# Kernel tuning notes

Measured on AMD Instinct MI355X. Metric: run time of the kernel, lower is better.

## Reference

```python
import jax, jax.numpy as jnp
import numpy as np

N_NODES = 100000


def gcn_conv(x, W, b, src, dst, n_nodes):
    """PyG GCNConv: out = D^{-1/2} (A + I) D^{-1/2} X W + b."""
    h = x @ W  # [N, F_out]
    # add self-loops
    loop = jnp.arange(n_nodes, dtype=src.dtype)
    s = jnp.concatenate([src, loop])
    d = jnp.concatenate([dst, loop])
    # symmetric normalization (deg counts incoming edges incl. self-loop)
    deg = jax.ops.segment_sum(jnp.ones_like(d, dtype=h.dtype), d, num_segments=n_nodes)
    dinv = jnp.where(deg > 0, jax.lax.rsqrt(deg), 0.0)
    coef = dinv[s] * dinv[d]  # [E+N]
    msg = h[s] * coef[:, None]  # gather + scale
    out = jax.ops.segment_sum(msg, d, num_segments=n_nodes)  # scatter-add
    return out + b


def setup_inputs() -> dict:
    key = jax.random.key(0)
    k1, k2, k3, k4, k5, k6 = jax.random.split(key, 6)
    in_dim, hidden_dim, out_dim = 128, 64, 64
    n_edges = 1000000
    x = jax.random.normal(k1, (N_NODES, in_dim), dtype=jnp.float32)
    edge_index = jax.random.randint(k2, (2, n_edges), 0, N_NODES, dtype=jnp.int64)
    # glorot-style init for GCN weights
    W1 = jax.random.normal(k3, (in_dim, hidden_dim), dtype=jnp.float32) / np.sqrt(in_dim)
    b1 = jnp.zeros((hidden_dim,), dtype=jnp.float32)
    W2 = jax.random.normal(k4, (hidden_dim, out_dim), dtype=jnp.float32) / np.sqrt(hidden_dim)
    b2 = jnp.zeros((out_dim,), dtype=jnp.float32)
    return {"x": x, "edge_index": edge_index, "W1": W1, "b1": b1, "W2": W2, "b2": b2}


def reference(x, edge_index, W1, b1, W2, b2):
    src, dst = edge_index[0], edge_index[1]
    h = jax.nn.relu(gcn_conv(x, W1, b1, src, dst, N_NODES))
    out = gcn_conv(h, W2, b2, src, dst, N_NODES)
    return out
```

## Files before the change

kernel.cpp:

```cpp
#include <hip/hip_runtime.h>


#define MD 48
#define FILLB 8192

typedef __attribute__((ext_vector_type(8))) short bf16x8;
typedef __attribute__((ext_vector_type(4))) float f32x4;
typedef __attribute__((ext_vector_type(4))) int   i32x4;
typedef __attribute__((ext_vector_type(4))) unsigned u32x4;

__device__ inline float bf2f(unsigned short v) {
    unsigned u = (unsigned)v << 16;
    return __builtin_bit_cast(float, u);
}
__device__ inline unsigned short f2bf(float f) {
    unsigned u = __builtin_bit_cast(unsigned, f);
    unsigned r = (u + 0x7FFFu + ((u >> 16) & 1u)) >> 16;
    return (unsigned short)r;
}

__device__ inline void convW_one(const float* __restrict__ W, short* __restrict__ Wth,
                                 short* __restrict__ Wtl, int K, int k, int f) {
    float v = W[k * 64 + f];
    unsigned b = __builtin_bit_cast(unsigned, v);
    unsigned hb = b & 0xFFFF0000u;
    float d = v - __builtin_bit_cast(float, hb);
    unsigned lb = __builtin_bit_cast(unsigned, d);
    Wth[f * K + k] = (short)(hb >> 16);
    Wtl[f * K + k] = (short)(lb >> 16);
}

__global__ __launch_bounds__(256) void k_prep(int* __restrict__ cnt, int n, int nbz,
                                              const float* __restrict__ W1,
                                              short* __restrict__ W1th, short* __restrict__ W1tl,
                                              const float* __restrict__ W2,
                                              short* __restrict__ W2th, short* __restrict__ W2tl) {
    const int b = blockIdx.x;
    if (b < nbz) {
        int i = b * 256 + threadIdx.x;
        if (i < n) cnt[i] = 0;
    } else if (b < nbz + 128) {
        if (threadIdx.x < 64) convW_one(W1, W1th, W1tl, 128, b - nbz, threadIdx.x);
    } else {
        if (threadIdx.x < 64) convW_one(W2, W2th, W2tl, 64, b - nbz - 128, threadIdx.x);
    }
}

template <int K>
__device__ inline void mm_f32A_body(int bid, const float* __restrict__ X,
                                    const short* __restrict__ Wth,
                                    const short* __restrict__ Wtl,
                                    unsigned short* __restrict__ G, int n) {
    const int lane = threadIdx.x & 63;
    const int w = threadIdx.x >> 6;
    const int r0 = lane & 15;
    const int kq = lane >> 4;
    const int arow = bid * 64 + w * 16 + r0;
    const float* xrow = X + (size_t)(arow < n ? arow : n - 1) * K;

    f32x4 acc[4] = {};
#pragma unroll
    for (int kc = 0; kc < K / 32; ++kc) {
        const int ks = kc * 32 + kq * 8;
        float xv[8];
        *(f32x4*)&xv[0] = __builtin_nontemporal_load((const f32x4*)&xrow[ks]);
        *(f32x4*)&xv[4] = __builtin_nontemporal_load((const f32x4*)&xrow[ks + 4]);
        bf16x8 ah, al;
#pragma unroll
        for (int j = 0; j < 8; ++j) {
            unsigned b = __builtin_bit_cast(unsigned, xv[j]);
            unsigned hb = b & 0xFFFF0000u;
            float d = xv[j] - __builtin_bit_cast(float, hb);
            unsigned lb = __builtin_bit_cast(unsigned, d);
            ah[j] = (short)(hb >> 16);
            al[j] = (short)(lb >> 16);
        }
#pragma unroll
        for (int c = 0; c < 4; ++c) {
            bf16x8 bh = *(const bf16x8*)&Wth[(c * 16 + r0) * K + ks];
            bf16x8 bl = *(const bf16x8*)&Wtl[(c * 16 + r0) * K + ks];
            acc[c] = __builtin_amdgcn_mfma_f32_16x16x32_bf16(ah, bh, acc[c], 0, 0, 0);
            acc[c] = __builtin_amdgcn_mfma_f32_16x16x32_bf16(ah, bl, acc[c], 0, 0, 0);
            acc[c] = __builtin_amdgcn_mfma_f32_16x16x32_bf16(al, bh, acc[c], 0, 0, 0);
        }
    }
    const int orow = bid * 64 + w * 16 + kq * 4;
#pragma unroll
    for (int rg = 0; rg < 4; ++rg) {
        int gr = orow + rg;
        if (gr < n) {
#pragma unroll
            for (int c = 0; c < 4; ++c)
                G[(size_t)gr * 64 + c * 16 + r0] = f2bf(acc[c][rg]);
        }
    }
}

template <int K>
__global__ __launch_bounds__(256) void k_fill_mm1(const int* __restrict__ src,
                                                  const int* __restrict__ dst, int E,
                                                  int* __restrict__ cnt,
                                                  int* __restrict__ col_ell, int npx,
                                                  const float* __restrict__ X,
                                                  const short* __restrict__ Wth,
                                                  const short* __restrict__ Wtl,
                                                  unsigned short* __restrict__ G, int n) {
    if (blockIdx.x < FILLB) {
        const int myxcd = blockIdx.x & 7;
        const int lo = myxcd * npx;
        const int hi = lo + npx;
        const int vb = blockIdx.x >> 3;
        const int nvb = FILLB >> 3;
        const int tid = vb * 256 + threadIdx.x;
        const int nthr = nvb * 256;
        for (int base = tid * 4; base < E; base += nthr * 4) {
            i32x4 d4 = __builtin_nontemporal_load((const i32x4*)&dst[base]);
#pragma unroll
            for (int k = 0; k < 4; ++k) {
                int d = d4[k];
                if (d >= lo && d < hi) {
                    int p = atomicAdd(&cnt[d], 1);
                    if (p < MD)
                        col_ell[(size_t)d * MD + p] = __builtin_nontemporal_load(&src[base + k]);
                }
            }
        }
    } else {
        mm_f32A_body<K>(blockIdx.x - FILLB, X, Wth, Wtl, G, n);
    }
}

__global__ __launch_bounds__(256) void k_mm_bf16A(const unsigned short* __restrict__ A,
                                                  const short* __restrict__ Wth,
                                                  const short* __restrict__ Wtl,
                                                  unsigned short* __restrict__ G, int n) {
    constexpr int K = 64;
    const int lane = threadIdx.x & 63;
    const int w = threadIdx.x >> 6;
    const int r0 = lane & 15;
    const int kq = lane >> 4;
    const int arow = blockIdx.x * 64 + w * 16 + r0;
    const unsigned short* ar = A + (size_t)(arow < n ? arow : n - 1) * K;

    f32x4 acc[4] = {};
#pragma unroll
    for (int kc = 0; kc < K / 32; ++kc) {
        const int ks = kc * 32 + kq * 8;
        bf16x8 a = __builtin_nontemporal_load((const bf16x8*)&ar[ks]);
#pragma unroll
        for (int c = 0; c < 4; ++c) {
            bf16x8 bh = *(const bf16x8*)&Wth[(c * 16 + r0) * K + ks];
            bf16x8 bl = *(const bf16x8*)&Wtl[(c * 16 + r0) * K + ks];
            acc[c] = __builtin_amdgcn_mfma_f32_16x16x32_bf16(a, bh, acc[c], 0, 0, 0);
            acc[c] = __builtin_amdgcn_mfma_f32_16x16x32_bf16(a, bl, acc[c], 0, 0, 0);
        }
    }
    const int orow = blockIdx.x * 64 + w * 16 + kq * 4;
#pragma unroll
    for (int rg = 0; rg < 4; ++rg) {
        int gr = orow + rg;
        if (gr < n) {
#pragma unroll
            for (int c = 0; c < 4; ++c)
                G[(size_t)gr * 64 + c * 16 + r0] = f2bf(acc[c][rg]);
        }
    }
}

template <bool RELU, bool OUTBF>
__global__ __launch_bounds__(256) void k_gather8(const unsigned short* __restrict__ g,
                                                 const int* __restrict__ cntArr,
                                                 const int* __restrict__ col_ell,
                                                 const float* __restrict__ bias,
                                                 void* __restrict__ dest, int n) {
    const int node = blockIdx.x * 4 + (threadIdx.x >> 6);
    if (node >= n) return;
    const int lane = threadIdx.x & 63;
    const int grp = lane >> 3;
    const int fl = lane & 7;
    const int cn = cntArr[node];
    const int lc = min(cn, MD);
    const float dn = rsqrtf((float)(cn + 1));
    const int myidx = __builtin_nontemporal_load(&col_ell[(size_t)node * MD + lane]);
    const int vidx = (lane < lc) ? myidx : node;
    const float mydv = rsqrtf((float)(cntArr[vidx] + 1));

    float acc[8] = {};
    if (grp == 0) {
        u32x4 u = *(const u32x4*)&g[(size_t)node * 64 + fl * 8];
        acc[0] = dn * bf2f((unsigned short)(u[0] & 0xFFFF));
        acc[1] = dn * bf2f((unsigned short)(u[0] >> 16));
        acc[2] = dn * bf2f((unsigned short)(u[1] & 0xFFFF));
        acc[3] = dn * bf2f((unsigned short)(u[1] >> 16));
        acc[4] = dn * bf2f((unsigned short)(u[2] & 0xFFFF));
        acc[5] = dn * bf2f((unsigned short)(u[2] >> 16));
        acc[6] = dn * bf2f((unsigned short)(u[3] & 0xFFFF));
        acc[7] = dn * bf2f((unsigned short)(u[3] >> 16));
    }
    for (int j8 = 0; j8 < lc; j8 += 8) {
        int j = j8 + grp;
        int s = __shfl(myidx, j);
        float ds = __shfl(mydv, j);
        if (j < lc) {
            u32x4 u = *(const u32x4*)&g[(size_t)s * 64 + fl * 8];
            acc[0] = fmaf(ds, bf2f((unsigned short)(u[0] & 0xFFFF)), acc[0]);
            acc[1] = fmaf(ds, bf2f((unsigned short)(u[0] >> 16)),    acc[1]);
            acc[2] = fmaf(ds, bf2f((unsigned short)(u[1] & 0xFFFF)), acc[2]);
            acc[3] = fmaf(ds, bf2f((unsigned short)(u[1] >> 16)),    acc[3]);
            acc[4] = fmaf(ds, bf2f((unsigned short)(u[2] & 0xFFFF)), acc[4]);
            acc[5] = fmaf(ds, bf2f((unsigned short)(u[2] >> 16)),    acc[5]);
            acc[6] = fmaf(ds, bf2f((unsigned short)(u[3] & 0xFFFF)), acc[6]);
            acc[7] = fmaf(ds, bf2f((unsigned short)(u[3] >> 16)),    acc[7]);
        }
    }
#pragma unroll
    for (int k = 0; k < 8; ++k) {
        acc[k] += __shfl_xor(acc[k], 8);
        acc[k] += __shfl_xor(acc[k], 16);
        acc[k] += __shfl_xor(acc[k], 32);
    }
    if (grp == 0) {
        float v[8];
        const float* bv = &bias[fl * 8];
#pragma unroll
        for (int k = 0; k < 8; ++k) {
            v[k] = fmaf(acc[k], dn, bv[k]);
            if (RELU) v[k] = fmaxf(v[k], 0.f);
        }
        if (OUTBF) {
            u32x4 o;
            o[0] = (unsigned)f2bf(v[0]) | ((unsigned)f2bf(v[1]) << 16);
            o[1] = (unsigned)f2bf(v[2]) | ((unsigned)f2bf(v[3]) << 16);
            o[2] = (unsigned)f2bf(v[4]) | ((unsigned)f2bf(v[5]) << 16);
            o[3] = (unsigned)f2bf(v[6]) | ((unsigned)f2bf(v[7]) << 16);
            __builtin_nontemporal_store(o, (u32x4*)&((unsigned short*)dest)[(size_t)node * 64 + fl * 8]);
        } else {
            float* dp = &((float*)dest)[(size_t)node * 64 + fl * 8];
            __builtin_nontemporal_store(*(const f32x4*)&v[0], (f32x4*)&dp[0]);
            __builtin_nontemporal_store(*(const f32x4*)&v[4], (f32x4*)&dp[4]);
        }
    }
}

extern "C" void kernel_launch(void* const* d_in, const int* in_sizes, int n_in,
                              void* d_out, int out_size, void* d_ws, size_t ws_size,
                              hipStream_t stream) {
    const float* x  = (const float*)d_in[0];
    const int*   ei = (const int*)d_in[1];
    const float* W1 = (const float*)d_in[2];
    const float* b1 = (const float*)d_in[3];
    const float* W2 = (const float*)d_in[4];
    const float* b2 = (const float*)d_in[5];

    const int N = in_sizes[0] / 128;
    const int E = in_sizes[1] / 2;
    const int* src = ei;
    const int* dst = ei + E;
    float* out = (float*)d_out;

    char* ws = (char*)d_ws;
    size_t off = 0;
    auto alloc = [&](size_t bytes) {
        void* p = ws + off;
        off += (bytes + 63) & ~(size_t)63;
        return p;
    };
    unsigned short* a1   = (unsigned short*)alloc((size_t)N * 64 * 2);
    unsigned short* gbuf = (unsigned short*)alloc((size_t)N * 64 * 2);
    int*   cnt     = (int*)alloc((size_t)N * 4);
    int*   col_ell = (int*)alloc(((size_t)N * MD + 64) * 4);
    short* W1th    = (short*)alloc((size_t)64 * 128 * 2);
    short* W1tl    = (short*)alloc((size_t)64 * 128 * 2);
    short* W2th    = (short*)alloc((size_t)64 * 64 * 2);
    short* W2tl    = (short*)alloc((size_t)64 * 64 * 2);

    const int NBZ   = (N + 255) / 256;
    const int NB_MM = (N + 63) / 64;
    const int NB_G  = (N + 3) / 4;
    const int npx   = (N + 7) / 8;

    k_prep<<<NBZ + 192, 256, 0, stream>>>(cnt, N, NBZ, W1, W1th, W1tl, W2, W2th, W2tl);

    k_fill_mm1<128><<<FILLB + NB_MM, 256, 0, stream>>>(src, dst, E, cnt, col_ell, npx,
                                                       x, W1th, W1tl, gbuf, N);

    k_gather8<true, true><<<NB_G, 256, 0, stream>>>(gbuf, cnt, col_ell, b1, a1, N);

    k_mm_bf16A<<<NB_MM, 256, 0, stream>>>(a1, W2th, W2tl, gbuf, N);
    k_gather8<false, false><<<NB_G, 256, 0, stream>>>(gbuf, cnt, col_ell, b2, out, N);
}
```

Before: 216.0 us.

## Fold source-side degree scaling into GEMM epilogue and split fill from GEMM

The GEMM epilogues now multiply each output row by rsqrt(deg+1), so the gathers no longer need a per-neighbour dinv lookup through a dependent cnt load and shuffle. They accumulate plain sums instead. Because the scaling needs the finished counts, the fused fill+GEMM launch is split into separate fill and GEMM kernels. That gives up the overlap of edge bucketing with the first matmul and adds a launch. Several nontemporal loads and stores were also switched to regular ones.

```diff
diff --git a/kernel.cpp b/kernel.cpp
--- a/kernel.cpp
+++ b/kernel.cpp
@@ -2,7 +2,6 @@
 
 
 #define MD 48
-#define FILLB 8192
 
 typedef __attribute__((ext_vector_type(8))) short bf16x8;
 typedef __attribute__((ext_vector_type(4))) float f32x4;
@@ -46,16 +45,41 @@
     }
 }
 
+__global__ __launch_bounds__(256) void k_fill_xcd(const int* __restrict__ src,
+                                                  const int* __restrict__ dst, int E,
+                                                  int* __restrict__ cnt,
+                                                  int* __restrict__ col_ell, int npx) {
+    const int myxcd = blockIdx.x & 7;
+    const int lo = myxcd * npx;
+    const int hi = lo + npx;
+    const int vb = blockIdx.x >> 3;
+    const int nvb = gridDim.x >> 3;
+    const int tid = vb * 256 + threadIdx.x;
+    const int nthr = nvb * 256;
+    for (int base = tid * 4; base < E; base += nthr * 4) {
+        i32x4 d4 = *(const i32x4*)&dst[base];
+#pragma unroll
+        for (int k = 0; k < 4; ++k) {
+            int d = d4[k];
+            if (d >= lo && d < hi) {
+                int p = atomicAdd(&cnt[d], 1);
+                if (p < MD) col_ell[(size_t)d * MD + p] = src[base + k];
+            }
+        }
+    }
+}
+
 template <int K>
-__device__ inline void mm_f32A_body(int bid, const float* __restrict__ X,
-                                    const short* __restrict__ Wth,
-                                    const short* __restrict__ Wtl,
-                                    unsigned short* __restrict__ G, int n) {
+__global__ __launch_bounds__(256) void k_mm_f32A(const float* __restrict__ X,
+                                                 const short* __restrict__ Wth,
+                                                 const short* __restrict__ Wtl,
+                                                 const int* __restrict__ cnt,
+                                                 unsigned short* __restrict__ G, int n) {
     const int lane = threadIdx.x & 63;
     const int w = threadIdx.x >> 6;
     const int r0 = lane & 15;
     const int kq = lane >> 4;
-    const int arow = bid * 64 + w * 16 + r0;
+    const int arow = blockIdx.x * 64 + w * 16 + r0;
     const float* xrow = X + (size_t)(arow < n ? arow : n - 1) * K;
 
     f32x4 acc[4] = {};
@@ -84,55 +108,23 @@
             acc[c] = __builtin_amdgcn_mfma_f32_16x16x32_bf16(al, bh, acc[c], 0, 0, 0);
         }
     }
-    const int orow = bid * 64 + w * 16 + kq * 4;
+    const int orow = blockIdx.x * 64 + w * 16 + kq * 4;
 #pragma unroll
     for (int rg = 0; rg < 4; ++rg) {
         int gr = orow + rg;
         if (gr < n) {
+            float di = rsqrtf((float)(cnt[gr] + 1));
 #pragma unroll
             for (int c = 0; c < 4; ++c)
-                G[(size_t)gr * 64 + c * 16 + r0] = f2bf(acc[c][rg]);
-        }
-    }
-}
-
-template <int K>
-__global__ __launch_bounds__(256) void k_fill_mm1(const int* __restrict__ src,
-                                                  const int* __restrict__ dst, int E,
-                                                  int* __restrict__ cnt,
-                                                  int* __restrict__ col_ell, int npx,
-                                                  const float* __restrict__ X,
-                                                  const short* __restrict__ Wth,
-                                                  const short* __restrict__ Wtl,
-                                                  unsigned short* __restrict__ G, int n) {
-    if (blockIdx.x < FILLB) {
-        const int myxcd = blockIdx.x & 7;
-        const int lo = myxcd * npx;
-        const int hi = lo + npx;
-        const int vb = blockIdx.x >> 3;
-        const int nvb = FILLB >> 3;
-        const int tid = vb * 256 + threadIdx.x;
-        const int nthr = nvb * 256;
-        for (int base = tid * 4; base < E; base += nthr * 4) {
-            i32x4 d4 = __builtin_nontemporal_load((const i32x4*)&dst[base]);
-#pragma unroll
-            for (int k = 0; k < 4; ++k) {
-                int d = d4[k];
-                if (d >= lo && d < hi) {
-                    int p = atomicAdd(&cnt[d], 1);
-                    if (p < MD)
-                        col_ell[(size_t)d * MD + p] = __builtin_nontemporal_load(&src[base + k]);
-                }
-            }
-        }
-    } else {
-        mm_f32A_body<K>(blockIdx.x - FILLB, X, Wth, Wtl, G, n);
+                G[(size_t)gr * 64 + c * 16 + r0] = f2bf(acc[c][rg] * di);
+        }
     }
 }
 
 __global__ __launch_bounds__(256) void k_mm_bf16A(const unsigned short* __restrict__ A,
                                                   const short* __restrict__ Wth,
                                                   const short* __restrict__ Wtl,
+                                                  const int* __restrict__ cnt,
                                                   unsigned short* __restrict__ G, int n) {
     constexpr int K = 64;
     const int lane = threadIdx.x & 63;
@@ -160,9 +152,10 @@
     for (int rg = 0; rg < 4; ++rg) {
         int gr = orow + rg;
         if (gr < n) {
+            float di = rsqrtf((float)(cnt[gr] + 1));
 #pragma unroll
             for (int c = 0; c < 4; ++c)
-                G[(size_t)gr * 64 + c * 16 + r0] = f2bf(acc[c][rg]);
+                G[(size_t)gr * 64 + c * 16 + r0] = f2bf(acc[c][rg] * di);
         }
     }
 }
@@ -181,36 +174,27 @@
     const int cn = cntArr[node];
     const int lc = min(cn, MD);
     const float dn = rsqrtf((float)(cn + 1));
-    const int myidx = __builtin_nontemporal_load(&col_ell[(size_t)node * MD + lane]);
-    const int vidx = (lane < lc) ? myidx : node;
-    const float mydv = rsqrtf((float)(cntArr[vidx] + 1));
+    const int myidx = col_ell[(size_t)node * MD + lane];
 
     float acc[8] = {};
     if (grp == 0) {
         u32x4 u = *(const u32x4*)&g[(size_t)node * 64 + fl * 8];
-        acc[0] = dn * bf2f((unsigned short)(u[0] & 0xFFFF));
-        acc[1] = dn * bf2f((unsigned short)(u[0] >> 16));
-        acc[2] = dn * bf2f((unsigned short)(u[1] & 0xFFFF));
-        acc[3] = dn * bf2f((unsigned short)(u[1] >> 16));
-        acc[4] = dn * bf2f((unsigned short)(u[2] & 0xFFFF));
-        acc[5] = dn * bf2f((unsigned short)(u[2] >> 16));
-        acc[6] = dn * bf2f((unsigned short)(u[3] & 0xFFFF));
-        acc[7] = dn * bf2f((unsigned short)(u[3] >> 16));
+#pragma unroll
+        for (int k = 0; k < 4; ++k) {
+            acc[2 * k]     = bf2f((unsigned short)(u[k] & 0xFFFF));
+            acc[2 * k + 1] = bf2f((unsigned short)(u[k] >> 16));
+        }
     }
     for (int j8 = 0; j8 < lc; j8 += 8) {
         int j = j8 + grp;
         int s = __shfl(myidx, j);
-        float ds = __shfl(mydv, j);
         if (j < lc) {
             u32x4 u = *(const u32x4*)&g[(size_t)s * 64 + fl * 8];
-            acc[0] = fmaf(ds, bf2f((unsigned short)(u[0] & 0xFFFF)), acc[0]);
-            acc[1] = fmaf(ds, bf2f((unsigned short)(u[0] >> 16)),    acc[1]);
-            acc[2] = fmaf(ds, bf2f((unsigned short)(u[1] & 0xFFFF)), acc[2]);
-            acc[3] = fmaf(ds, bf2f((unsigned short)(u[1] >> 16)),    acc[3]);
-            acc[4] = fmaf(ds, bf2f((unsigned short)(u[2] & 0xFFFF)), acc[4]);
-            acc[5] = fmaf(ds, bf2f((unsigned short)(u[2] >> 16)),    acc[5]);
-            acc[6] = fmaf(ds, bf2f((unsigned short)(u[3] & 0xFFFF)), acc[6]);
-            acc[7] = fmaf(ds, bf2f((unsigned short)(u[3] >> 16)),    acc[7]);
+#pragma unroll
+            for (int k = 0; k < 4; ++k) {
+                acc[2 * k]     += bf2f((unsigned short)(u[k] & 0xFFFF));
+                acc[2 * k + 1] += bf2f((unsigned short)(u[k] >> 16));
+            }
         }
     }
 #pragma unroll
@@ -233,7 +217,7 @@
             o[1] = (unsigned)f2bf(v[2]) | ((unsigned)f2bf(v[3]) << 16);
             o[2] = (unsigned)f2bf(v[4]) | ((unsigned)f2bf(v[5]) << 16);
             o[3] = (unsigned)f2bf(v[6]) | ((unsigned)f2bf(v[7]) << 16);
-            __builtin_nontemporal_store(o, (u32x4*)&((unsigned short*)dest)[(size_t)node * 64 + fl * 8]);
+            *(u32x4*)&((unsigned short*)dest)[(size_t)node * 64 + fl * 8] = o;
         } else {
             float* dp = &((float*)dest)[(size_t)node * 64 + fl * 8];
             __builtin_nontemporal_store(*(const f32x4*)&v[0], (f32x4*)&dp[0]);
@@ -281,11 +265,11 @@
 
     k_prep<<<NBZ + 192, 256, 0, stream>>>(cnt, N, NBZ, W1, W1th, W1tl, W2, W2th, W2tl);
 
-    k_fill_mm1<128><<<FILLB + NB_MM, 256, 0, stream>>>(src, dst, E, cnt, col_ell, npx,
-                                                       x, W1th, W1tl, gbuf, N);
-
+    k_fill_xcd<<<8192, 256, 0, stream>>>(src, dst, E, cnt, col_ell, npx);
+
+    k_mm_f32A<128><<<NB_MM, 256, 0, stream>>>(x, W1th, W1tl, cnt, gbuf, N);
     k_gather8<true, true><<<NB_G, 256, 0, stream>>>(gbuf, cnt, col_ell, b1, a1, N);
 
-    k_mm_bf16A<<<NB_MM, 256, 0, stream>>>(a1, W2th, W2tl, gbuf, N);
+    k_mm_bf16A<<<NB_MM, 256, 0, stream>>>(a1, W2th, W2tl, cnt, gbuf, N);
     k_gather8<false, false><<<NB_G, 256, 0, stream>>>(gbuf, cnt, col_ell, b2, out, N);
 }
```

Result: faster. 187.1 us (-13.4%).
